# Performance work log

Hardware: AMD Instinct MI355X
Metric: run time of the kernel (lower is better)

## Reference

```python
import jax, jax.numpy as jnp
import numpy as np
from jax import lax

B, T, K = 4096, 512, 7


def setup_inputs() -> dict:
    key = jax.random.key(0)
    k1, k2, k3, k4, k5, k6 = jax.random.split(key, 6)
    emissions = jax.random.normal(k1, (B, T, K), dtype=jnp.float32)
    # variable-length sequences: mask is a contiguous prefix of ones (token_ids.gt(0))
    lengths = jax.random.randint(k2, (B,), T // 2, T + 1)
    mask = (jnp.arange(T)[None, :] < lengths[:, None]).astype(jnp.int32)
    tags = jax.random.randint(k3, (B, T), 0, K).astype(jnp.int64)
    transitions = jax.random.normal(k4, (K, K), dtype=jnp.float32) * 0.1
    start_transitions = jax.random.normal(k5, (K,), dtype=jnp.float32) * 0.1
    end_transitions = jax.random.normal(k6, (K,), dtype=jnp.float32) * 0.1
    return {
        "emissions": emissions,
        "mask": mask,
        "tags": tags,
        "transitions": transitions,
        "start_transitions": start_transitions,
        "end_transitions": end_transitions,
    }


def _crf_nll(emissions, mask, tags, transitions, start_transitions, end_transitions):
    maskf = mask.astype(emissions.dtype)  # [B, T]
    # ---- numerator: score of the gold path ----
    em_tag = jnp.take_along_axis(emissions, tags[..., None], axis=2)[..., 0]  # [B, T]
    score = start_transitions[tags[:, 0]] + em_tag[:, 0]  # [B]
    trans_score = transitions[tags[:, :-1], tags[:, 1:]]  # [B, T-1]
    score = score + jnp.sum((trans_score + em_tag[:, 1:]) * maskf[:, 1:], axis=1)
    last_idx = jnp.sum(mask, axis=1).astype(jnp.int32) - 1  # [B]
    last_tag = jnp.take_along_axis(tags, last_idx[:, None].astype(tags.dtype), axis=1)[:, 0]
    score = score + end_transitions[last_tag]
    # ---- denominator: log partition via forward algorithm (stable logsumexp DP) ----
    alpha0 = start_transitions[None, :] + emissions[:, 0]  # [B, K]

    def step(alpha, xs):
        em_t, m_t = xs  # [B, K], [B]
        # alpha[b, i] + transitions[i, j] + em_t[b, j] -> logsumexp over i
        nxt = jax.nn.logsumexp(alpha[:, :, None] + transitions[None, :, :] + em_t[:, None, :], axis=1)
        alpha = jnp.where(m_t[:, None] > 0, nxt, alpha)
        return alpha, None

    xs = (jnp.swapaxes(emissions[:, 1:], 0, 1), jnp.swapaxes(mask[:, 1:], 0, 1))  # [T-1, B, K], [T-1, B]
    alpha, _ = lax.scan(step, alpha0, xs)
    log_z = jax.nn.logsumexp(alpha + end_transitions[None, :], axis=1)  # [B]
    return jnp.mean(log_z - score)


def reference(emissions, mask, tags, transitions, start_transitions, end_transitions):
    return _crf_nll(emissions, mask, tags, transitions, start_transitions, end_transitions)
```

## Files before the change

kernel.cpp:

```cpp
#include <hip/hip_runtime.h>

#define BB 4096
#define TT 512
#define KK 7
#define NC 32
#define SS 16

__device__ __forceinline__ float fexp2(float x){ float r; asm("v_exp_f32 %0, %1" : "=v"(r) : "v"(x)); return r; }
__device__ __forceinline__ float flog2(float x){ float r; asm("v_log_f32 %0, %1" : "=v"(r) : "v"(x)); return r; }

__global__ __launch_bounds__(256) void crf_p1(
    const float* __restrict__ em, const int* __restrict__ msk,
    const int* __restrict__ tgs, const float* __restrict__ trn,
    const float* __restrict__ stt,
    float* __restrict__ wsA, float* __restrict__ wsP,
    float* __restrict__ wsS, int* __restrict__ wsC)
{
  const float L2E = 1.44269504088896340736f;
  int tid = blockIdx.x * 256 + threadIdx.x;
  int c = tid >> 12;
  int b = tid & (BB - 1);

  float e2[KK*KK];
  #pragma unroll
  for (int i = 0; i < KK*KK; i++) e2[i] = fexp2(trn[i] * L2E);

  float sc = 0.f; int cnt = 0;
  const size_t ebase = (size_t)b * TT * KK;

  if (c == 0) {
    float u[KK], Ls;
    float a2[KK];
    #pragma unroll
    for (int j = 0; j < KK; j++) a2[j] = (stt[j] + em[ebase + j]) * L2E;
    float m = a2[0];
    #pragma unroll
    for (int j = 1; j < KK; j++) m = fmaxf(m, a2[j]);
    #pragma unroll
    for (int j = 0; j < KK; j++) u[j] = fexp2(a2[j] - m);
    Ls = m;
    cnt = msk[b * TT];
    int tprev = tgs[b * TT];
    float en_[KK]; int mkn, tgn;
    #pragma unroll
    for (int k = 0; k < KK; k++) en_[k] = em[ebase + KK + k];
    mkn = msk[b * TT + 1]; tgn = tgs[b * TT + 1];

    for (int t = 1; t < SS; ++t) {
      float e_[KK];
      #pragma unroll
      for (int k = 0; k < KK; k++) e_[k] = en_[k];
      int mk = mkn, tg = tgn;
      if (!mk) break;
      int t2 = (t + 1 < TT) ? t + 1 : TT - 1;
      #pragma unroll
      for (int k = 0; k < KK; k++) en_[k] = em[ebase + (size_t)t2 * KK + k];
      mkn = msk[b * TT + t2]; tgn = tgs[b * TT + t2];
      float es = e_[0];
      #pragma unroll
      for (int k = 1; k < KK; k++) es = (tg == k) ? e_[k] : es;
      sc += trn[tprev * KK + tg] + es;
      tprev = tg; cnt++;
      float g[KK];
      #pragma unroll
      for (int j = 0; j < KK; j++) g[j] = fexp2(e_[j] * L2E);
      float acc[KK];
      #pragma unroll
      for (int j = 0; j < KK; j++) acc[j] = u[0] * e2[j];
      #pragma unroll
      for (int k = 1; k < KK; k++)
        #pragma unroll
        for (int j = 0; j < KK; j++) acc[j] = fmaf(u[k], e2[k*KK + j], acc[j]);
      #pragma unroll
      for (int j = 0; j < KK; j++) u[j] = acc[j] * g[j];
      if ((cnt & 3) == 0) {
        float mm = u[0];
        #pragma unroll
        for (int j = 1; j < KK; j++) mm = fmaxf(mm, u[j]);
        int ex = (int)((__float_as_uint(mm) >> 23) & 255) - 127;
        float scl = __uint_as_float((unsigned)(127 - ex) << 23);
        Ls += (float)ex;
        #pragma unroll
        for (int j = 0; j < KK; j++) u[j] *= scl;
      }
    }
    #pragma unroll
    for (int j = 0; j < KK; j++) wsA[b * 8 + j] = Ls + flog2(u[j]);
    wsS[b] = sc; wsC[b] = cnt;
  } else {
    int t0 = c * SS;
    float R[KK*KK], Lr[KK];
    #pragma unroll
    for (int i = 0; i < KK*KK; i++) R[i] = 0.f;
    #pragma unroll
    for (int i = 0; i < KK; i++) { R[i*KK + i] = 1.f; Lr[i] = 0.f; }
    int tprev = tgs[b * TT + t0 - 1];
    float en_[KK]; int mkn, tgn;
    #pragma unroll
    for (int k = 0; k < KK; k++) en_[k] = em[ebase + (size_t)t0 * KK + k];
    mkn = msk[b * TT + t0]; tgn = tgs[b * TT + t0];

    for (int t = t0; t < t0 + SS; ++t) {
      float e_[KK];
      #pragma unroll
      for (int k = 0; k < KK; k++) e_[k] = en_[k];
      int mk = mkn, tg = tgn;
      if (!mk) break;
      int t2 = (t + 1 < TT) ? t + 1 : TT - 1;
      #pragma unroll
      for (int k = 0; k < KK; k++) en_[k] = em[ebase + (size_t)t2 * KK + k];
      mkn = msk[b * TT + t2]; tgn = tgs[b * TT + t2];
      float es = e_[0];
      #pragma unroll
      for (int k = 1; k < KK; k++) es = (tg == k) ? e_[k] : es;
      sc += trn[tprev * KK + tg] + es;
      tprev = tg; cnt++;
      float g[KK];
      #pragma unroll
      for (int j = 0; j < KK; j++) g[j] = fexp2(e_[j] * L2E);
      #pragma unroll
      for (int i = 0; i < KK; i++) {
        float acc[KK];
        #pragma unroll
        for (int j = 0; j < KK; j++) acc[j] = R[i*KK] * e2[j];
        #pragma unroll
        for (int k = 1; k < KK; k++)
          #pragma unroll
          for (int j = 0; j < KK; j++) acc[j] = fmaf(R[i*KK + k], e2[k*KK + j], acc[j]);
        #pragma unroll
        for (int j = 0; j < KK; j++) R[i*KK + j] = acc[j] * g[j];
      }
      if ((cnt & 3) == 0) {
        #pragma unroll
        for (int i = 0; i < KK; i++) {
          float mm = R[i*KK];
          #pragma unroll
          for (int j = 1; j < KK; j++) mm = fmaxf(mm, R[i*KK + j]);
          int ex = (int)((__float_as_uint(mm) >> 23) & 255) - 127;
          float scl = __uint_as_float((unsigned)(127 - ex) << 23);
          Lr[i] += (float)ex;
          #pragma unroll
          for (int j = 0; j < KK; j++) R[i*KK + j] *= scl;
        }
      }
    }
    wsS[c * BB + b] = sc; wsC[c * BB + b] = cnt;
    if (cnt > 0) {
      float* P = wsP + ((size_t)(c - 1) * BB + b) * 49;
      #pragma unroll
      for (int i = 0; i < KK; i++)
        #pragma unroll
        for (int j = 0; j < KK; j++) P[i*KK + j] = Lr[i] + flog2(R[i*KK + j]);
    }
  }
}

__global__ __launch_bounds__(256) void crf_p2(
    const float* __restrict__ em, const int* __restrict__ tgs,
    const float* __restrict__ stt, const float* __restrict__ ent,
    const float* __restrict__ wsA, const float* __restrict__ wsP,
    const float* __restrict__ wsS, const int* __restrict__ wsC,
    float* __restrict__ out)
{
  const float L2E = 1.44269504088896340736f;
  const float LN2 = 0.69314718055994530942f;
  __shared__ float sm[4];
  int w = threadIdx.x >> 6, lane = threadIdx.x & 63;
  int b = blockIdx.x * 4 + w;

  int cntv = 0; float scv = 0.f;
  if (lane < NC) { cntv = wsC[lane * BB + b]; scv = wsS[lane * BB + b]; }
  int len = cntv; float ssum = scv;
  #pragma unroll
  for (int o = 1; o < 64; o <<= 1) { len += __shfl_xor(len, o); ssum += __shfl_xor(ssum, o); }

  float A = (lane < KK) ? wsA[b * 8 + lane] : -1e30f;
  int j = (lane < KK) ? lane : 0;
  for (int c2 = 1; c2 < NC; c2++) {
    int cc = __shfl(cntv, c2);
    if (cc == 0) break;
    const float* P = wsP + ((size_t)(c2 - 1) * BB + b) * 49;
    float v[KK];
    #pragma unroll
    for (int i = 0; i < KK; i++) v[i] = __shfl(A, i) + P[i*KK + j];
    float m = v[0];
    #pragma unroll
    for (int i = 1; i < KK; i++) m = fmaxf(m, v[i]);
    float s = 0.f;
    #pragma unroll
    for (int i = 0; i < KK; i++) s += fexp2(v[i] - m);
    A = m + flog2(s);
  }
  float x = (lane < KK) ? A + ent[lane] * L2E : -1e30f;
  float mx = x;
  #pragma unroll
  for (int o = 1; o < 8; o <<= 1) mx = fmaxf(mx, __shfl_xor(mx, o));
  float s = fexp2(x - mx);
  #pragma unroll
  for (int o = 1; o < 8; o <<= 1) s += __shfl_xor(s, o);

  if (lane == 0) {
    float logz = LN2 * (mx + flog2(s));
    int t0g = tgs[b * TT];
    float score = stt[t0g] + em[(size_t)b * TT * KK + t0g] + ssum
                + ent[tgs[b * TT + len - 1]];
    sm[w] = (logz - score) * (1.0f / BB);
  }
  __syncthreads();
  if (threadIdx.x == 0) atomicAdd(out, sm[0] + sm[1] + sm[2] + sm[3]);
}

extern "C" void kernel_launch(void* const* d_in, const int* in_sizes, int n_in,
                              void* d_out, int out_size, void* d_ws, size_t ws_size,
                              hipStream_t stream) {
  const float* em  = (const float*)d_in[0];
  const int*   msk = (const int*)d_in[1];
  const int*   tgs = (const int*)d_in[2];
  const float* trn = (const float*)d_in[3];
  const float* stt = (const float*)d_in[4];
  const float* ent = (const float*)d_in[5];
  float* out = (float*)d_out;

  float* wsA = (float*)d_ws;
  float* wsP = wsA + (size_t)BB * 8;
  float* wsS = wsP + (size_t)(NC - 1) * BB * 49;
  int*   wsC = (int*)(wsS + (size_t)NC * BB);

  hipMemsetAsync(out, 0, sizeof(float), stream);
  hipLaunchKernelGGL(crf_p1, dim3(BB * NC / 256), dim3(256), 0, stream,
                     em, msk, tgs, trn, stt, wsA, wsP, wsS, wsC);
  hipLaunchKernelGGL(crf_p2, dim3(BB / 4), dim3(256), 0, stream,
                     em, tgs, stt, ent, wsA, wsP, wsS, wsC, out);
}
```

Before: 174.7 us.

## Split chunk transfer matrices per row across threads and move gold score to p2

Phase 1 now gives each thread one row of a chunk's 7x7 transfer matrix instead of the whole matrix. This multiplies thread count by seven and shrinks per-thread register state. Emissions and mask are loaded as float4/int4 blocks, and the exp'd transition table is made wave-uniform with readfirstlane. The gold-path score and length are now computed in phase 2 with wave-parallel vectorized reads, which removes the wsS/wsC workspace; the chunk combine loop prefetches the next P matrix. The cost is seven-fold redundant emission loads and exps across the row threads.

```diff
diff --git a/kernel.cpp b/kernel.cpp
--- a/kernel.cpp
+++ b/kernel.cpp
@@ -3,163 +3,151 @@
 #define BB 4096
 #define TT 512
 #define KK 7
-#define NC 32
 #define SS 16
+#define NMAT (BB * 31 * 7)
 
 __device__ __forceinline__ float fexp2(float x){ float r; asm("v_exp_f32 %0, %1" : "=v"(r) : "v"(x)); return r; }
 __device__ __forceinline__ float flog2(float x){ float r; asm("v_log_f32 %0, %1" : "=v"(r) : "v"(x)); return r; }
+__device__ __forceinline__ float uni(float x){ return __int_as_float(__builtin_amdgcn_readfirstlane(__float_as_int(x))); }
 
 __global__ __launch_bounds__(256) void crf_p1(
     const float* __restrict__ em, const int* __restrict__ msk,
-    const int* __restrict__ tgs, const float* __restrict__ trn,
-    const float* __restrict__ stt,
-    float* __restrict__ wsA, float* __restrict__ wsP,
-    float* __restrict__ wsS, int* __restrict__ wsC)
+    const float* __restrict__ trn, const float* __restrict__ stt,
+    float* __restrict__ wsA, float* __restrict__ wsP)
 {
   const float L2E = 1.44269504088896340736f;
   int tid = blockIdx.x * 256 + threadIdx.x;
-  int c = tid >> 12;
-  int b = tid & (BB - 1);
-
-  float e2[KK*KK];
-  #pragma unroll
-  for (int i = 0; i < KK*KK; i++) e2[i] = fexp2(trn[i] * L2E);
-
-  float sc = 0.f; int cnt = 0;
-  const size_t ebase = (size_t)b * TT * KK;
-
-  if (c == 0) {
-    float u[KK], Ls;
-    float a2[KK];
-    #pragma unroll
-    for (int j = 0; j < KK; j++) a2[j] = (stt[j] + em[ebase + j]) * L2E;
-    float m = a2[0];
-    #pragma unroll
-    for (int j = 1; j < KK; j++) m = fmaxf(m, a2[j]);
-    #pragma unroll
-    for (int j = 0; j < KK; j++) u[j] = fexp2(a2[j] - m);
-    Ls = m;
-    cnt = msk[b * TT];
-    int tprev = tgs[b * TT];
-    float en_[KK]; int mkn, tgn;
-    #pragma unroll
-    for (int k = 0; k < KK; k++) en_[k] = em[ebase + KK + k];
-    mkn = msk[b * TT + 1]; tgn = tgs[b * TT + 1];
-
-    for (int t = 1; t < SS; ++t) {
-      float e_[KK];
-      #pragma unroll
-      for (int k = 0; k < KK; k++) e_[k] = en_[k];
-      int mk = mkn, tg = tgn;
-      if (!mk) break;
-      int t2 = (t + 1 < TT) ? t + 1 : TT - 1;
-      #pragma unroll
-      for (int k = 0; k < KK; k++) en_[k] = em[ebase + (size_t)t2 * KK + k];
-      mkn = msk[b * TT + t2]; tgn = tgs[b * TT + t2];
-      float es = e_[0];
-      #pragma unroll
-      for (int k = 1; k < KK; k++) es = (tg == k) ? e_[k] : es;
-      sc += trn[tprev * KK + tg] + es;
-      tprev = tg; cnt++;
-      float g[KK];
-      #pragma unroll
-      for (int j = 0; j < KK; j++) g[j] = fexp2(e_[j] * L2E);
-      float acc[KK];
-      #pragma unroll
-      for (int j = 0; j < KK; j++) acc[j] = u[0] * e2[j];
-      #pragma unroll
-      for (int k = 1; k < KK; k++)
-        #pragma unroll
-        for (int j = 0; j < KK; j++) acc[j] = fmaf(u[k], e2[k*KK + j], acc[j]);
-      #pragma unroll
-      for (int j = 0; j < KK; j++) u[j] = acc[j] * g[j];
-      if ((cnt & 3) == 0) {
-        float mm = u[0];
-        #pragma unroll
-        for (int j = 1; j < KK; j++) mm = fmaxf(mm, u[j]);
-        int ex = (int)((__float_as_uint(mm) >> 23) & 255) - 127;
-        float scl = __uint_as_float((unsigned)(127 - ex) << 23);
-        Ls += (float)ex;
-        #pragma unroll
-        for (int j = 0; j < KK; j++) u[j] *= scl;
-      }
-    }
-    #pragma unroll
-    for (int j = 0; j < KK; j++) wsA[b * 8 + j] = Ls + flog2(u[j]);
-    wsS[b] = sc; wsC[b] = cnt;
-  } else {
+
+  float e2[49];
+  #pragma unroll
+  for (int i = 0; i < 49; i++) e2[i] = uni(fexp2(trn[i] * L2E));
+
+  if (tid < NMAT) {
+    int q = tid / 7, i = tid - q * 7;
+    int b = q / 31, c = q - b * 31 + 1;
     int t0 = c * SS;
-    float R[KK*KK], Lr[KK];
-    #pragma unroll
-    for (int i = 0; i < KK*KK; i++) R[i] = 0.f;
-    #pragma unroll
-    for (int i = 0; i < KK; i++) { R[i*KK + i] = 1.f; Lr[i] = 0.f; }
-    int tprev = tgs[b * TT + t0 - 1];
-    float en_[KK]; int mkn, tgn;
-    #pragma unroll
-    for (int k = 0; k < KK; k++) en_[k] = em[ebase + (size_t)t0 * KK + k];
-    mkn = msk[b * TT + t0]; tgn = tgs[b * TT + t0];
-
-    for (int t = t0; t < t0 + SS; ++t) {
-      float e_[KK];
-      #pragma unroll
-      for (int k = 0; k < KK; k++) e_[k] = en_[k];
-      int mk = mkn, tg = tgn;
-      if (!mk) break;
-      int t2 = (t + 1 < TT) ? t + 1 : TT - 1;
-      #pragma unroll
-      for (int k = 0; k < KK; k++) en_[k] = em[ebase + (size_t)t2 * KK + k];
-      mkn = msk[b * TT + t2]; tgn = tgs[b * TT + t2];
-      float es = e_[0];
-      #pragma unroll
-      for (int k = 1; k < KK; k++) es = (tg == k) ? e_[k] : es;
-      sc += trn[tprev * KK + tg] + es;
-      tprev = tg; cnt++;
-      float g[KK];
-      #pragma unroll
-      for (int j = 0; j < KK; j++) g[j] = fexp2(e_[j] * L2E);
-      #pragma unroll
-      for (int i = 0; i < KK; i++) {
+    const size_t eb = (size_t)b * (TT * KK);
+
+    float R[KK];
+    #pragma unroll
+    for (int j = 0; j < KK; j++) R[j] = (j == i) ? 1.f : 0.f;
+    float Lr = 0.f; int cnt = 0; int alive = 1;
+
+    for (int g = 0; g < 4; g++) {
+      if (!alive) break;
+      int t = t0 + 4 * g;
+      float em_[28];
+      #pragma unroll
+      for (int p = 0; p < 7; p++) {
+        float4 f = *(const float4*)(em + eb + (size_t)t * KK + 4 * p);
+        em_[4*p+0] = f.x; em_[4*p+1] = f.y; em_[4*p+2] = f.z; em_[4*p+3] = f.w;
+      }
+      int4 m4 = *(const int4*)(msk + b * TT + t);
+      int ms[4] = {m4.x, m4.y, m4.z, m4.w};
+      #pragma unroll
+      for (int s = 0; s < 4; s++) {
+        if (!ms[s]) { alive = 0; break; }
+        cnt++;
         float acc[KK];
         #pragma unroll
-        for (int j = 0; j < KK; j++) acc[j] = R[i*KK] * e2[j];
+        for (int j = 0; j < KK; j++) acc[j] = R[0] * e2[j];
         #pragma unroll
         for (int k = 1; k < KK; k++)
           #pragma unroll
-          for (int j = 0; j < KK; j++) acc[j] = fmaf(R[i*KK + k], e2[k*KK + j], acc[j]);
-        #pragma unroll
-        for (int j = 0; j < KK; j++) R[i*KK + j] = acc[j] * g[j];
-      }
-      if ((cnt & 3) == 0) {
-        #pragma unroll
-        for (int i = 0; i < KK; i++) {
-          float mm = R[i*KK];
-          #pragma unroll
-          for (int j = 1; j < KK; j++) mm = fmaxf(mm, R[i*KK + j]);
+          for (int j = 0; j < KK; j++) acc[j] = fmaf(R[k], e2[k*KK + j], acc[j]);
+        #pragma unroll
+        for (int j = 0; j < KK; j++) R[j] = acc[j] * fexp2(em_[s*KK + j] * L2E);
+        if ((cnt & 3) == 0) {
+          float mm = R[0];
+          #pragma unroll
+          for (int j = 1; j < KK; j++) mm = fmaxf(mm, R[j]);
           int ex = (int)((__float_as_uint(mm) >> 23) & 255) - 127;
           float scl = __uint_as_float((unsigned)(127 - ex) << 23);
-          Lr[i] += (float)ex;
-          #pragma unroll
-          for (int j = 0; j < KK; j++) R[i*KK + j] *= scl;
+          Lr += (float)ex;
+          #pragma unroll
+          for (int j = 0; j < KK; j++) R[j] *= scl;
         }
       }
     }
-    wsS[c * BB + b] = sc; wsC[c * BB + b] = cnt;
     if (cnt > 0) {
-      float* P = wsP + ((size_t)(c - 1) * BB + b) * 49;
-      #pragma unroll
-      for (int i = 0; i < KK; i++)
-        #pragma unroll
-        for (int j = 0; j < KK; j++) P[i*KK + j] = Lr[i] + flog2(R[i*KK + j]);
-    }
+      float* P = wsP + ((size_t)(c - 1) * BB + b) * 49 + i * KK;
+      #pragma unroll
+      for (int j = 0; j < KK; j++) P[j] = Lr + flog2(R[j]);
+    }
+  } else {
+    int b = tid - NMAT;
+    const size_t eb = (size_t)b * (TT * KK);
+    float em_[28];
+    #pragma unroll
+    for (int p = 0; p < 7; p++) {
+      float4 f = *(const float4*)(em + eb + 4 * p);
+      em_[4*p+0] = f.x; em_[4*p+1] = f.y; em_[4*p+2] = f.z; em_[4*p+3] = f.w;
+    }
+    int4 m4 = *(const int4*)(msk + b * TT);
+    int ms[4] = {m4.x, m4.y, m4.z, m4.w};
+
+    float u[KK], Ls;
+    {
+      float a2[KK];
+      #pragma unroll
+      for (int j = 0; j < KK; j++) a2[j] = (stt[j] + em_[j]) * L2E;
+      float m = a2[0];
+      #pragma unroll
+      for (int j = 1; j < KK; j++) m = fmaxf(m, a2[j]);
+      #pragma unroll
+      for (int j = 0; j < KK; j++) u[j] = fexp2(a2[j] - m);
+      Ls = m;
+    }
+    int cnt = ms[0]; int alive = 1;
+
+    for (int g = 0; g < 4; g++) {
+      if (g > 0) {
+        if (!alive) break;
+        int t = 4 * g;
+        #pragma unroll
+        for (int p = 0; p < 7; p++) {
+          float4 f = *(const float4*)(em + eb + (size_t)t * KK + 4 * p);
+          em_[4*p+0] = f.x; em_[4*p+1] = f.y; em_[4*p+2] = f.z; em_[4*p+3] = f.w;
+        }
+        int4 n4 = *(const int4*)(msk + b * TT + t);
+        ms[0] = n4.x; ms[1] = n4.y; ms[2] = n4.z; ms[3] = n4.w;
+      }
+      #pragma unroll
+      for (int s = 0; s < 4; s++) {
+        if (g == 0 && s == 0) continue;
+        if (!ms[s]) { alive = 0; break; }
+        cnt++;
+        float acc[KK];
+        #pragma unroll
+        for (int j = 0; j < KK; j++) acc[j] = u[0] * e2[j];
+        #pragma unroll
+        for (int k = 1; k < KK; k++)
+          #pragma unroll
+          for (int j = 0; j < KK; j++) acc[j] = fmaf(u[k], e2[k*KK + j], acc[j]);
+        #pragma unroll
+        for (int j = 0; j < KK; j++) u[j] = acc[j] * fexp2(em_[s*KK + j] * L2E);
+        if ((cnt & 3) == 0) {
+          float mm = u[0];
+          #pragma unroll
+          for (int j = 1; j < KK; j++) mm = fmaxf(mm, u[j]);
+          int ex = (int)((__float_as_uint(mm) >> 23) & 255) - 127;
+          float scl = __uint_as_float((unsigned)(127 - ex) << 23);
+          Ls += (float)ex;
+          #pragma unroll
+          for (int j = 0; j < KK; j++) u[j] *= scl;
+        }
+      }
+    }
+    #pragma unroll
+    for (int j = 0; j < KK; j++) wsA[b * 8 + j] = Ls + flog2(u[j]);
   }
 }
 
 __global__ __launch_bounds__(256) void crf_p2(
-    const float* __restrict__ em, const int* __restrict__ tgs,
+    const float* __restrict__ em, const int* __restrict__ msk,
+    const int* __restrict__ tgs, const float* __restrict__ trn,
     const float* __restrict__ stt, const float* __restrict__ ent,
     const float* __restrict__ wsA, const float* __restrict__ wsP,
-    const float* __restrict__ wsS, const int* __restrict__ wsC,
     float* __restrict__ out)
 {
   const float L2E = 1.44269504088896340736f;
@@ -167,43 +155,73 @@
   __shared__ float sm[4];
   int w = threadIdx.x >> 6, lane = threadIdx.x & 63;
   int b = blockIdx.x * 4 + w;
-
-  int cntv = 0; float scv = 0.f;
-  if (lane < NC) { cntv = wsC[lane * BB + b]; scv = wsS[lane * BB + b]; }
-  int len = cntv; float ssum = scv;
-  #pragma unroll
-  for (int o = 1; o < 64; o <<= 1) { len += __shfl_xor(len, o); ssum += __shfl_xor(ssum, o); }
+  const int* mrow = msk + b * TT;
+  const int* trow = tgs + b * TT;
+  const size_t eb = (size_t)b * (TT * KK);
+
+  int4 ma = *(const int4*)(mrow + lane * 8);
+  int4 mb = *(const int4*)(mrow + lane * 8 + 4);
+  int len = ma.x + ma.y + ma.z + ma.w + mb.x + mb.y + mb.z + mb.w;
+  #pragma unroll
+  for (int o = 1; o < 64; o <<= 1) len += __shfl_xor(len, o);
+
+  int4 ta = *(const int4*)(trow + lane * 8);
+  int4 tb = *(const int4*)(trow + lane * 8 + 4);
+  int tga[8] = {ta.x, ta.y, ta.z, ta.w, tb.x, tb.y, tb.z, tb.w};
+  int tprev = lane ? trow[lane * 8 - 1] : 0;
+  float scp = 0.f;
+  #pragma unroll
+  for (int s = 0; s < 8; s++) {
+    int t = lane * 8 + s; int tg = tga[s];
+    if (t == 0)          scp += stt[tg] + em[eb + tg];
+    else if (t < len)    scp += trn[tprev * KK + tg] + em[eb + (size_t)t * KK + tg];
+    if (t == len - 1)    scp += ent[tg];
+    tprev = tg;
+  }
+  float score = scp;
+  #pragma unroll
+  for (int o = 1; o < 64; o <<= 1) score += __shfl_xor(score, o);
 
   float A = (lane < KK) ? wsA[b * 8 + lane] : -1e30f;
   int j = (lane < KK) ? lane : 0;
-  for (int c2 = 1; c2 < NC; c2++) {
-    int cc = __shfl(cntv, c2);
-    if (cc == 0) break;
-    const float* P = wsP + ((size_t)(c2 - 1) * BB + b) * 49;
+  int nact = (len - 1) >> 4; if (nact > 31) nact = 31;
+  const float* Pb = wsP + (size_t)b * 49;
+  const size_t cs = (size_t)BB * 49;
+  float cur[KK];
+  if (nact >= 1) {
+    #pragma unroll
+    for (int i = 0; i < KK; i++) cur[i] = Pb[i * KK + j];
+  }
+  for (int c2 = 1; c2 <= nact; c2++) {
+    float nxt[KK];
+    if (c2 < nact) {
+      #pragma unroll
+      for (int i = 0; i < KK; i++) nxt[i] = Pb[(size_t)c2 * cs + i * KK + j];
+    }
     float v[KK];
     #pragma unroll
-    for (int i = 0; i < KK; i++) v[i] = __shfl(A, i) + P[i*KK + j];
+    for (int i = 0; i < KK; i++) v[i] = __shfl(A, i) + cur[i];
     float m = v[0];
     #pragma unroll
     for (int i = 1; i < KK; i++) m = fmaxf(m, v[i]);
-    float s = 0.f;
-    #pragma unroll
-    for (int i = 0; i < KK; i++) s += fexp2(v[i] - m);
-    A = m + flog2(s);
-  }
+    float ssum = 0.f;
+    #pragma unroll
+    for (int i = 0; i < KK; i++) ssum += fexp2(v[i] - m);
+    A = m + flog2(ssum);
+    #pragma unroll
+    for (int i = 0; i < KK; i++) cur[i] = nxt[i];
+  }
+
   float x = (lane < KK) ? A + ent[lane] * L2E : -1e30f;
   float mx = x;
   #pragma unroll
   for (int o = 1; o < 8; o <<= 1) mx = fmaxf(mx, __shfl_xor(mx, o));
-  float s = fexp2(x - mx);
-  #pragma unroll
-  for (int o = 1; o < 8; o <<= 1) s += __shfl_xor(s, o);
+  float se = fexp2(x - mx);
+  #pragma unroll
+  for (int o = 1; o < 8; o <<= 1) se += __shfl_xor(se, o);
 
   if (lane == 0) {
-    float logz = LN2 * (mx + flog2(s));
-    int t0g = tgs[b * TT];
-    float score = stt[t0g] + em[(size_t)b * TT * KK + t0g] + ssum
-                + ent[tgs[b * TT + len - 1]];
+    float logz = LN2 * (mx + flog2(se));
     sm[w] = (logz - score) * (1.0f / BB);
   }
   __syncthreads();
@@ -223,12 +241,10 @@
 
   float* wsA = (float*)d_ws;
   float* wsP = wsA + (size_t)BB * 8;
-  float* wsS = wsP + (size_t)(NC - 1) * BB * 49;
-  int*   wsC = (int*)(wsS + (size_t)NC * BB);
 
   hipMemsetAsync(out, 0, sizeof(float), stream);
-  hipLaunchKernelGGL(crf_p1, dim3(BB * NC / 256), dim3(256), 0, stream,
-                     em, msk, tgs, trn, stt, wsA, wsP, wsS, wsC);
+  hipLaunchKernelGGL(crf_p1, dim3((NMAT + BB) / 256), dim3(256), 0, stream,
+                     em, msk, trn, stt, wsA, wsP);
   hipLaunchKernelGGL(crf_p2, dim3(BB / 4), dim3(256), 0, stream,
-                     em, tgs, stt, ent, wsA, wsP, wsS, wsC, out);
+                     em, msk, tgs, trn, stt, ent, wsA, wsP, out);
 }
```

Result: slower. 179.7 us (+2.9%).
